# Kernel tuning notes

Hardware: AMD Instinct MI355X
Metric: run time of the kernel (lower is better)

The kernel has to match this reference:

```python
import jax, jax.numpy as jnp
import numpy as np

N, E, G = 50000, 800000, 64
IN_CH, HID, HEADS, NUM_CLASSES = 128, 64, 4, 10
NEG_SLOPE = 0.2


def _gat_conv(x, src, dst, W, a_src, a_dst, b, concat):
    """PyG-style GATConv with default add_self_loops=True (inference mode)."""
    n = x.shape[0]
    H, C = a_src.shape
    h = (x @ W).reshape(n, H, C)                       # [N,H,C]
    loop = jnp.arange(n, dtype=src.dtype)
    si = jnp.concatenate([src, loop])                  # [E+N]
    di = jnp.concatenate([dst, loop])
    as_n = jnp.sum(h * a_src, axis=-1)                 # [N,H]
    ad_n = jnp.sum(h * a_dst, axis=-1)                 # [N,H]
    e = jax.nn.leaky_relu(as_n[si] + ad_n[di], NEG_SLOPE)   # [E+N,H]
    m = jax.ops.segment_max(e, di, num_segments=n)     # segment softmax (stable)
    ex = jnp.exp(e - m[di])
    denom = jax.ops.segment_sum(ex, di, num_segments=n)
    alpha = ex / (denom[di] + 1e-16)                   # [E+N,H]
    out = jax.ops.segment_sum(alpha[:, :, None] * h[si], di, num_segments=n)  # [N,H,C]
    out = out.reshape(n, H * C) if concat else out.mean(axis=1)
    return out + b


def setup_inputs() -> dict:
    key = jax.random.key(0)
    ks = jax.random.split(key, 20)
    d = {}
    d["x"] = jax.random.normal(ks[0], (N, IN_CH), dtype=jnp.float32)
    d["src"] = jax.random.randint(ks[1], (E,), 0, N, dtype=jnp.int32)
    d["dst"] = jax.random.randint(ks[2], (E,), 0, N, dtype=jnp.int32)
    d["batch"] = jnp.sort(jax.random.randint(ks[3], (N,), 0, G, dtype=jnp.int32))
    s = 0.1
    d["W1"] = jax.random.normal(ks[4], (IN_CH, HEADS * HID), dtype=jnp.float32) * s
    d["as1"] = jax.random.normal(ks[5], (HEADS, HID), dtype=jnp.float32) * s
    d["ad1"] = jax.random.normal(ks[6], (HEADS, HID), dtype=jnp.float32) * s
    d["b1"] = jnp.zeros((HEADS * HID,), jnp.float32)
    d["W2"] = jax.random.normal(ks[7], (HEADS * HID, HEADS * HID), dtype=jnp.float32) * s
    d["as2"] = jax.random.normal(ks[8], (HEADS, HID), dtype=jnp.float32) * s
    d["ad2"] = jax.random.normal(ks[9], (HEADS, HID), dtype=jnp.float32) * s
    d["b2"] = jnp.zeros((HEADS * HID,), jnp.float32)
    # proj: 256 -> 64, heads=1, concat=False
    d["Wp"] = jax.random.normal(ks[10], (HEADS * HID, HID), dtype=jnp.float32) * s
    d["asp"] = jax.random.normal(ks[11], (1, HID), dtype=jnp.float32) * s
    d["adp"] = jax.random.normal(ks[12], (1, HID), dtype=jnp.float32) * s
    d["bp"] = jnp.zeros((HID,), jnp.float32)
    # MLP head
    d["Wh1"] = jax.random.normal(ks[13], (HID, HID), dtype=jnp.float32) * s
    d["bh1"] = jnp.zeros((HID,), jnp.float32)
    d["Wh2"] = jax.random.normal(ks[14], (HID, NUM_CLASSES), dtype=jnp.float32) * s
    d["bh2"] = jnp.zeros((NUM_CLASSES,), jnp.float32)
    return d


def reference(x, src, dst, batch, W1, as1, ad1, b1, W2, as2, ad2, b2,
              Wp, asp, adp, bp, Wh1, bh1, Wh2, bh2):
    h = jax.nn.elu(_gat_conv(x, src, dst, W1, as1, ad1, b1, concat=True))
    h = jax.nn.elu(_gat_conv(h, src, dst, W2, as2, ad2, b2, concat=True))
    h = jax.nn.elu(_gat_conv(h, src, dst, Wp, asp, adp, bp, concat=False))  # [N,HID]
    # global mean pool over graphs
    sums = jax.ops.segment_sum(h, batch, num_segments=G)                    # [G,HID]
    cnt = jax.ops.segment_sum(jnp.ones((h.shape[0],), h.dtype), batch, num_segments=G)
    g = sums / jnp.maximum(cnt, 1.0)[:, None]
    z = jax.nn.relu(g @ Wh1 + bh1)
    return z @ Wh2 + bh2                                                    # [G,NUM_CLASSES]
```

## Files before the change

### kernel.cpp

```cpp
#include <hip/hip_runtime.h>
#include <hip/hip_fp16.h>
#include <cstdint>
#include <cstddef>

#define NNODES 50000
#define NEDGES 800000
#define NGRAPH 64
#define BCAP 128

typedef __attribute__((ext_vector_type(8))) _Float16 half8;
typedef __attribute__((ext_vector_type(4))) float float4v;

__device__ __forceinline__ float lrelu(float x) { return x > 0.f ? x : 0.2f * x; }

__device__ __forceinline__ void wtrans_elem(const float* __restrict__ W,
                                            _Float16* __restrict__ Wt,
                                            int K, int N, int i) {
    int k = i / N, n = i - k * N;
    Wt[(size_t)n * K + k] = (_Float16)W[i];
}

__global__ void prep(const float* __restrict__ W1, const float* __restrict__ W2,
                     const float* __restrict__ Wp, _Float16* __restrict__ w1t,
                     _Float16* __restrict__ w2t, _Float16* __restrict__ wpt,
                     int* __restrict__ cnt) {
    int i = blockIdx.x * blockDim.x + threadIdx.x;
    if (i < 32768) wtrans_elem(W1, w1t, 128, 256, i);
    else if (i < 98304) wtrans_elem(W2, w2t, 256, 256, i - 32768);
    else if (i < 114688) wtrans_elem(Wp, wpt, 256, 64, i - 98304);
    else if (i < 114688 + NNODES) cnt[i - 114688] = 0;
}

__global__ __launch_bounds__(256) void scatter(const int* __restrict__ src,
                                               const int* __restrict__ dst,
                                               int* __restrict__ cnt,
                                               int* __restrict__ bucket) {
    int e = blockIdx.x * 256 + threadIdx.x;
    if (e < NEDGES) {
        int d = dst[e];
        int pos = atomicAdd(&cnt[d], 1);
        if (pos < BCAP) bucket[(size_t)d * BCAP + pos] = src[e];
    }
}

template <int KD, int NFB, int NTOT, int HTOT, bool F32A>
__global__ __launch_bounds__(512) void gemm_lds(const _Float16* __restrict__ A,
                                                const float* __restrict__ A32,
                                                const _Float16* __restrict__ Wt,
                                                const float* __restrict__ a_src,
                                                const float* __restrict__ a_dst,
                                                _Float16* __restrict__ C,
                                                float* __restrict__ as_n,
                                                float* __restrict__ ad_n,
                                                int M) {
    constexpr int NSPLIT = NTOT / (NFB * 16);
    constexpr int HLOC = NFB / 4;
    constexpr int KT = KD / 32;
    constexpr int KC = KD / 8;
    extern __shared__ _Float16 bsm[];

    const int bm = blockIdx.x / NSPLIT;
    const int bn = blockIdx.x % NSPLIT;
    const int tid = threadIdx.x;
    const int w = tid >> 6;
    const int lane = tid & 63;
    const int quad = lane >> 4;
    const int mcol = lane & 15;

    int arow = bm * 128 + w * 16 + mcol;
    if (arow >= M) arow = M - 1;

    half8 areg[KT];
    if constexpr (F32A) {
        const float* ap = A32 + (size_t)arow * KD + quad * 8;
#pragma unroll
        for (int i = 0; i < KT; ++i) {
            float4 t0 = *reinterpret_cast<const float4*>(ap + i * 32);
            float4 t1 = *reinterpret_cast<const float4*>(ap + i * 32 + 4);
            areg[i][0] = (_Float16)t0.x; areg[i][1] = (_Float16)t0.y;
            areg[i][2] = (_Float16)t0.z; areg[i][3] = (_Float16)t0.w;
            areg[i][4] = (_Float16)t1.x; areg[i][5] = (_Float16)t1.y;
            areg[i][6] = (_Float16)t1.z; areg[i][7] = (_Float16)t1.w;
        }
    } else {
        const _Float16* ap = A + (size_t)arow * KD + quad * 8;
#pragma unroll
        for (int i = 0; i < KT; ++i)
            areg[i] = *reinterpret_cast<const half8*>(ap + i * 32);
    }

    constexpr int CHUNKS = NFB * 16 * KC;
    const _Float16* wb = Wt + (size_t)bn * NFB * 16 * KD;
#pragma unroll
    for (int it = 0; it < CHUNKS / 512; ++it) {
        int idx = it * 512 + tid;
        int n = idx / KC, c = idx % KC;
        half8 v = *reinterpret_cast<const half8*>(wb + (size_t)n * KD + c * 8);
        *reinterpret_cast<half8*>(&bsm[n * KD + ((c ^ (n & 7)) * 8)]) = v;
    }
    __syncthreads();

    float4v acc[NFB];
#pragma unroll
    for (int nf = 0; nf < NFB; ++nf) acc[nf] = (float4v)0.f;
#pragma unroll
    for (int i = 0; i < KT; ++i) {
#pragma unroll
        for (int nf = 0; nf < NFB; ++nf) {
            int n = nf * 16 + mcol;
            int ch = (quad + i * 4) ^ (n & 7);
            half8 b = *reinterpret_cast<const half8*>(&bsm[n * KD + ch * 8]);
            acc[nf] = __builtin_amdgcn_mfma_f32_16x16x32_f16(areg[i], b, acc[nf], 0, 0, 0);
        }
    }

    const int orow0 = bm * 128 + w * 16 + quad * 4;
    const int cbase = bn * NFB * 16 + mcol;
#pragma unroll
    for (int r = 0; r < 4; ++r) {
        int orow = orow0 + r;
        if (orow < M) {
            _Float16* crow = C + (size_t)orow * NTOT + cbase;
#pragma unroll
            for (int nf = 0; nf < NFB; ++nf) crow[nf * 16] = (_Float16)acc[nf][r];
        }
    }

    float ps[HLOC][4], pd[HLOC][4];
#pragma unroll
    for (int hd = 0; hd < HLOC; ++hd)
#pragma unroll
        for (int r = 0; r < 4; ++r) { ps[hd][r] = 0.f; pd[hd][r] = 0.f; }
#pragma unroll
    for (int nf = 0; nf < NFB; ++nf) {
        float asv = a_src[bn * NFB * 16 + nf * 16 + mcol];
        float adv = a_dst[bn * NFB * 16 + nf * 16 + mcol];
#pragma unroll
        for (int r = 0; r < 4; ++r) {
            ps[nf >> 2][r] = fmaf(acc[nf][r], asv, ps[nf >> 2][r]);
            pd[nf >> 2][r] = fmaf(acc[nf][r], adv, pd[nf >> 2][r]);
        }
    }
#pragma unroll
    for (int off = 1; off < 16; off <<= 1) {
#pragma unroll
        for (int hd = 0; hd < HLOC; ++hd)
#pragma unroll
            for (int r = 0; r < 4; ++r) {
                ps[hd][r] += __shfl_xor(ps[hd][r], off);
                pd[hd][r] += __shfl_xor(pd[hd][r], off);
            }
    }
    if (mcol == 0) {
#pragma unroll
        for (int r = 0; r < 4; ++r) {
            int orow = orow0 + r;
            if (orow < M) {
#pragma unroll
                for (int hd = 0; hd < HLOC; ++hd) {
                    as_n[orow * HTOT + bn * HLOC + hd] = ps[hd][r];
                    ad_n[orow * HTOT + bn * HLOC + hd] = pd[hd][r];
                }
            }
        }
    }
}

__global__ __launch_bounds__(256) void node_agg2(const int* __restrict__ bucket,
                                                 const int* __restrict__ cnt,
                                                 const __half* __restrict__ h,
                                                 const float* __restrict__ asn,
                                                 const float* __restrict__ adn,
                                                 const float* __restrict__ bias,
                                                 _Float16* __restrict__ outp, int Nn) {
    constexpr int H = 4, HC = 256, EPC = 16;
    const int wid = blockIdx.x * 4 + (threadIdx.x >> 6);
    int n0 = wid * 2;
    if (n0 >= Nn) return;
    int n1 = n0 + 1;
    const bool has1 = (n1 < Nn);
    if (!has1) n1 = n0;
    const int lane = threadIdx.x & 63;
    const int hd = lane >> 4;
    const int ej = lane & 15;
    const int base = lane & 48;
    const int rs0 = n0 * BCAP, rs1 = n1 * BCAP;
    const int re0 = rs0 + min(cnt[n0], BCAP);
    const int re1 = rs1 + min(cnt[n1], BCAP);

    const float ad0 = adn[n0 * H + hd];
    const float ad1 = adn[n1 * H + hd];
    const float es0 = lrelu(asn[n0 * H + hd] + ad0);
    const float es1 = lrelu(asn[n1 * H + hd] + ad1);

    float m0 = es0, m1 = es1;
    float dp0 = (ej == 0) ? 1.f : 0.f;
    float dp1 = dp0;

    float a0, a1, a2, a3, b0, b1, b2, b3;
    {
        uint2 u = *reinterpret_cast<const uint2*>(&h[(size_t)n0 * HC + lane * 4]);
        float2 f0 = __half22float2(*reinterpret_cast<__half2*>(&u.x));
        float2 f1 = __half22float2(*reinterpret_cast<__half2*>(&u.y));
        a0 = f0.x; a1 = f0.y; a2 = f1.x; a3 = f1.y;
    }
    {
        uint2 u = *reinterpret_cast<const uint2*>(&h[(size_t)n1 * HC + lane * 4]);
        float2 f0 = __half22float2(*reinterpret_cast<__half2*>(&u.x));
        float2 f1 = __half22float2(*reinterpret_cast<__half2*>(&u.y));
        b0 = f0.x; b1 = f0.y; b2 = f1.x; b3 = f1.y;
    }

    int c0 = rs0, c1 = rs1;
    while (c0 < re0 || c1 < re1) {
        const int i0 = c0 + ej, i1 = c1 + ej;
        int s0v = 0, s1v = 0;
        float e0 = -1e30f, e1 = -1e30f;
        if (i0 < re0) s0v = bucket[i0];
        if (i1 < re1) s1v = bucket[i1];
        if (i0 < re0) e0 = lrelu(asn[s0v * H + hd] + ad0);
        if (i1 < re1) e1 = lrelu(asn[s1v * H + hd] + ad1);

        float cm0 = e0, cm1 = e1;
#pragma unroll
        for (int off = 1; off < EPC; off <<= 1) {
            cm0 = fmaxf(cm0, __shfl_xor(cm0, off));
            cm1 = fmaxf(cm1, __shfl_xor(cm1, off));
        }
        const float mn0 = fmaxf(m0, cm0);
        const float mn1 = fmaxf(m1, cm1);
        const float sc0 = __expf(m0 - mn0);
        const float sc1 = __expf(m1 - mn1);
        m0 = mn0; m1 = mn1;
        dp0 *= sc0; dp1 *= sc1;
        a0 *= sc0; a1 *= sc0; a2 *= sc0; a3 *= sc0;
        b0 *= sc1; b1 *= sc1; b2 *= sc1; b3 *= sc1;
        const float x0 = __expf(e0 - m0);
        const float x1 = __expf(e1 - m1);
        dp0 += x0; dp1 += x1;

        auto bodyA = [&](int j) {
            float ex = __shfl(x0, base + j);
            int sj = __shfl(s0v, base + j);
            uint2 u = *reinterpret_cast<const uint2*>(&h[(size_t)sj * HC + lane * 4]);
            float2 f0 = __half22float2(*reinterpret_cast<__half2*>(&u.x));
            float2 f1 = __half22float2(*reinterpret_cast<__half2*>(&u.y));
            a0 = fmaf(ex, f0.x, a0);
            a1 = fmaf(ex, f0.y, a1);
            a2 = fmaf(ex, f1.x, a2);
            a3 = fmaf(ex, f1.y, a3);
        };
        auto bodyB = [&](int j) {
            float ex = __shfl(x1, base + j);
            int sj = __shfl(s1v, base + j);
            uint2 u = *reinterpret_cast<const uint2*>(&h[(size_t)sj * HC + lane * 4]);
            float2 f0 = __half22float2(*reinterpret_cast<__half2*>(&u.x));
            float2 f1 = __half22float2(*reinterpret_cast<__half2*>(&u.y));
            b0 = fmaf(ex, f0.x, b0);
            b1 = fmaf(ex, f0.y, b1);
            b2 = fmaf(ex, f1.x, b2);
            b3 = fmaf(ex, f1.y, b3);
        };

        const int nA = min(EPC, re0 - c0);
        const int nB = min(EPC, re1 - c1);
        const int nmax = max(nA, nB);
        if (nmax == EPC) {
#pragma unroll
            for (int j = 0; j < EPC; ++j) { bodyA(j); bodyB(j); }
        } else {
#pragma unroll 4
            for (int j = 0; j < nmax; ++j) { bodyA(j); bodyB(j); }
        }
        c0 += EPC; c1 += EPC;
    }

#pragma unroll
    for (int off = 1; off < EPC; off <<= 1) {
        dp0 += __shfl_xor(dp0, off);
        dp1 += __shfl_xor(dp1, off);
    }
    const float inv0 = 1.f / (dp0 + 1e-16f);
    const float inv1 = 1.f / (dp1 + 1e-16f);

    {
        float v0 = a0 * inv0 + bias[lane * 4 + 0];
        float v1 = a1 * inv0 + bias[lane * 4 + 1];
        float v2 = a2 * inv0 + bias[lane * 4 + 2];
        float v3 = a3 * inv0 + bias[lane * 4 + 3];
        v0 = v0 > 0.f ? v0 : expm1f(v0);
        v1 = v1 > 0.f ? v1 : expm1f(v1);
        v2 = v2 > 0.f ? v2 : expm1f(v2);
        v3 = v3 > 0.f ? v3 : expm1f(v3);
        union { _Float16 h4[4]; uint2 u; } r;
        r.h4[0] = (_Float16)v0; r.h4[1] = (_Float16)v1;
        r.h4[2] = (_Float16)v2; r.h4[3] = (_Float16)v3;
        reinterpret_cast<uint2*>(outp + (size_t)n0 * HC)[lane] = r.u;
    }
    if (has1) {
        float v0 = b0 * inv1 + bias[lane * 4 + 0];
        float v1 = b1 * inv1 + bias[lane * 4 + 1];
        float v2 = b2 * inv1 + bias[lane * 4 + 2];
        float v3 = b3 * inv1 + bias[lane * 4 + 3];
        v0 = v0 > 0.f ? v0 : expm1f(v0);
        v1 = v1 > 0.f ? v1 : expm1f(v1);
        v2 = v2 > 0.f ? v2 : expm1f(v2);
        v3 = v3 > 0.f ? v3 : expm1f(v3);
        union { _Float16 h4[4]; uint2 u; } r;
        r.h4[0] = (_Float16)v0; r.h4[1] = (_Float16)v1;
        r.h4[2] = (_Float16)v2; r.h4[3] = (_Float16)v3;
        reinterpret_cast<uint2*>(outp + (size_t)n1 * HC)[lane] = r.u;
    }
}

__global__ __launch_bounds__(256) void node_aggP(const int* __restrict__ bucket,
                                                 const int* __restrict__ cnt,
                                                 const __half* __restrict__ h,
                                                 const float* __restrict__ asn,
                                                 const float* __restrict__ adn,
                                                 const float* __restrict__ bias,
                                                 _Float16* __restrict__ outp, int Nn) {
    constexpr int HC = 64, EPC = 16;
    const int wv = threadIdx.x >> 6;
    const int lane = threadIdx.x & 63;
    const int li = lane & 15;
    const int gb = lane & 48;
    const int n = blockIdx.x * 16 + wv * 4 + (lane >> 4);
    if (n >= Nn) return;

    const int rs = n * BCAP;
    const int re = rs + min(cnt[n], BCAP);
    const float ad = adn[n];
    float m = lrelu(asn[n] + ad);
    float dp = (li == 0) ? 1.f : 0.f;

    float a0, a1, a2, a3;
    {
        uint2 u = *reinterpret_cast<const uint2*>(&h[(size_t)n * HC + li * 4]);
        float2 f0 = __half22float2(*reinterpret_cast<__half2*>(&u.x));
        float2 f1 = __half22float2(*reinterpret_cast<__half2*>(&u.y));
        a0 = f0.x; a1 = f0.y; a2 = f1.x; a3 = f1.y;
    }

    auto body = [&](int j, float x, int sv) {
        float ex = __shfl(x, gb + j);
        int sj = __shfl(sv, gb + j);
        uint2 u = *reinterpret_cast<const uint2*>(&h[(size_t)sj * HC + li * 4]);
        float2 f0 = __half22float2(*reinterpret_cast<__half2*>(&u.x));
        float2 f1 = __half22float2(*reinterpret_cast<__half2*>(&u.y));
        a0 = fmaf(ex, f0.x, a0);
        a1 = fmaf(ex, f0.y, a1);
        a2 = fmaf(ex, f1.x, a2);
        a3 = fmaf(ex, f1.y, a3);
    };

    for (int c = rs; c < re; c += EPC) {
        int i = c + li;
        int sv = 0;
        float e = -1e30f;
        if (i < re) {
            sv = bucket[i];
            e = lrelu(asn[sv] + ad);
        }
        float cm = e;
#pragma unroll
        for (int off = 1; off < EPC; off <<= 1) cm = fmaxf(cm, __shfl_xor(cm, off));
        float mn = fmaxf(m, cm);
        float sc = __expf(m - mn);
        m = mn;
        dp *= sc;
        a0 *= sc; a1 *= sc; a2 *= sc; a3 *= sc;
        float x = __expf(e - m);
        dp += x;
        const int nb2 = min(EPC, re - c);
        if (nb2 == EPC) {
#pragma unroll
            for (int j = 0; j < EPC; ++j) body(j, x, sv);
        } else {
#pragma unroll 4
            for (int j = 0; j < nb2; ++j) body(j, x, sv);
        }
    }
#pragma unroll
    for (int off = 1; off < EPC; off <<= 1) dp += __shfl_xor(dp, off);
    const float inv = 1.f / (dp + 1e-16f);
    float v0 = a0 * inv + bias[li * 4 + 0];
    float v1 = a1 * inv + bias[li * 4 + 1];
    float v2 = a2 * inv + bias[li * 4 + 2];
    float v3 = a3 * inv + bias[li * 4 + 3];
    v0 = v0 > 0.f ? v0 : expm1f(v0);
    v1 = v1 > 0.f ? v1 : expm1f(v1);
    v2 = v2 > 0.f ? v2 : expm1f(v2);
    v3 = v3 > 0.f ? v3 : expm1f(v3);
    union { _Float16 h4[4]; uint2 u; } r;
    r.h4[0] = (_Float16)v0; r.h4[1] = (_Float16)v1;
    r.h4[2] = (_Float16)v2; r.h4[3] = (_Float16)v3;
    *reinterpret_cast<uint2*>(&outp[(size_t)n * HC + li * 4]) = r.u;
}

__global__ __launch_bounds__(256) void pool_mlp(const __half* __restrict__ feat,
                                                const int* __restrict__ batch,
                                                const float* __restrict__ Wh1,
                                                const float* __restrict__ bh1,
                                                const float* __restrict__ Wh2,
                                                const float* __restrict__ bh2,
                                                float* __restrict__ out, int Nn) {
    __shared__ float swsum[4][64];
    __shared__ float smean[64];
    __shared__ float shid[64];
    const int g = blockIdx.x;
    const int tid = threadIdx.x;
    const int lane = tid & 63;
    const int w = tid >> 6;
    int lo = 0, hi = Nn;
    while (lo < hi) { int mid = (lo + hi) >> 1; if (batch[mid] < g) lo = mid + 1; else hi = mid; }
    const int start = lo;
    hi = Nn;
    while (lo < hi) { int mid = (lo + hi) >> 1; if (batch[mid] < g + 1) lo = mid + 1; else hi = mid; }
    const int end = lo;
    float acc = 0.f;
    for (int n = start + w; n < end; n += 4) acc += __half2float(feat[(size_t)n * 64 + lane]);
    swsum[w][lane] = acc;
    __syncthreads();
    if (w == 0) {
        float s = swsum[0][lane] + swsum[1][lane] + swsum[2][lane] + swsum[3][lane];
        float c = (float)(end - start);
        c = c > 1.f ? c : 1.f;
        smean[lane] = s / c;
    }
    __syncthreads();
    if (tid < 64) {
        float a = bh1[tid];
        for (int k = 0; k < 64; ++k) a = fmaf(smean[k], Wh1[k * 64 + tid], a);
        shid[tid] = a > 0.f ? a : 0.f;
    }
    __syncthreads();
    if (tid < 10) {
        float a = bh2[tid];
        for (int k = 0; k < 64; ++k) a = fmaf(shid[k], Wh2[k * 10 + tid], a);
        out[g * 10 + tid] = a;
    }
}

extern "C" void kernel_launch(void* const* d_in, const int* in_sizes, int n_in,
                              void* d_out, int out_size, void* d_ws, size_t ws_size,
                              hipStream_t stream) {
    const float* x   = (const float*)d_in[0];
    const int* src   = (const int*)d_in[1];
    const int* dst   = (const int*)d_in[2];
    const int* batch = (const int*)d_in[3];
    const float* W1  = (const float*)d_in[4];
    const float* as1 = (const float*)d_in[5];
    const float* ad1 = (const float*)d_in[6];
    const float* b1  = (const float*)d_in[7];
    const float* W2  = (const float*)d_in[8];
    const float* as2 = (const float*)d_in[9];
    const float* ad2 = (const float*)d_in[10];
    const float* b2  = (const float*)d_in[11];
    const float* Wp  = (const float*)d_in[12];
    const float* asp = (const float*)d_in[13];
    const float* adp = (const float*)d_in[14];
    const float* bp  = (const float*)d_in[15];
    const float* Wh1 = (const float*)d_in[16];
    const float* bh1 = (const float*)d_in[17];
    const float* Wh2 = (const float*)d_in[18];
    const float* bh2 = (const float*)d_in[19];
    float* out = (float*)d_out;

    _Float16* hbase = (_Float16*)d_ws;
    const size_t NHC = (size_t)NNODES * 256;
    _Float16* ha16  = hbase;
    _Float16* hb16  = ha16 + NHC;
    _Float16* projh = hb16 + NHC;
    _Float16* w1t   = projh + (size_t)NNODES * 64;
    _Float16* w2t   = w1t + 256 * 128;
    _Float16* wpt   = w2t + 256 * 256;
    float* asn = (float*)(wpt + 64 * 256);
    float* adn = asn + (size_t)NNODES * 4;
    int* cnt    = (int*)(adn + (size_t)NNODES * 4);
    int* bucket = cnt + NNODES;

    const int gemmGrid = (NNODES + 127) / 128;
    const int scatGrid = (NEDGES + 255) / 256;
    const int agg2Grid = ((NNODES + 1) / 2 + 3) / 4;
    const int aggPGrid = (NNODES + 15) / 16;

    prep<<<(114688 + NNODES + 255) / 256, 256, 0, stream>>>(W1, W2, Wp, w1t, w2t, wpt, cnt);
    scatter<<<scatGrid, 256, 0, stream>>>(src, dst, cnt, bucket);
    gemm_lds<128, 16, 256, 4, true><<<gemmGrid, 512, 65536, stream>>>(
        nullptr, x, w1t, as1, ad1, ha16, asn, adn, NNODES);
    node_agg2<<<agg2Grid, 256, 0, stream>>>(bucket, cnt,
        (const __half*)ha16, asn, adn, b1, hb16, NNODES);
    gemm_lds<256, 8, 256, 4, false><<<gemmGrid * 2, 512, 65536, stream>>>(
        hb16, nullptr, w2t, as2, ad2, ha16, asn, adn, NNODES);
    node_agg2<<<agg2Grid, 256, 0, stream>>>(bucket, cnt,
        (const __half*)ha16, asn, adn, b2, hb16, NNODES);
    gemm_lds<256, 4, 64, 1, false><<<gemmGrid, 512, 32768, stream>>>(
        hb16, nullptr, wpt, asp, adp, ha16, asn, adn, NNODES);
    node_aggP<<<aggPGrid, 256, 0, stream>>>(bucket, cnt,
        (const __half*)ha16, asn, adn, bp, projh, NNODES);
    pool_mlp<<<NGRAPH, 256, 0, stream>>>((const __half*)projh, batch, Wh1, bh1, Wh2, bh2, out, NNODES);
}
```

Measured before the change: 440.7 us.

## Fuse scatter with weight prep and fuse final aggregation with mean pooling

Merges the weight transpose/convert into the edge-scatter kernel and replaces the cnt-zeroing pass with a memset that also clears a per-graph sum buffer. Fuses the graph mean-pool into the last aggregation kernel through LDS atomics per graph slot, then global atomics, so the fp16 projection output no longer has to be written and re-read. The MLP head then only divides the sums and applies the two layers. This saves a launch and a node-sized round trip, at the cost of fp32 atomics with order-dependent summation.

```diff
diff --git a/kernel.cpp b/kernel.cpp
--- a/kernel.cpp
+++ b/kernel.cpp
@@ -20,26 +20,30 @@
     Wt[(size_t)n * K + k] = (_Float16)W[i];
 }
 
-__global__ void prep(const float* __restrict__ W1, const float* __restrict__ W2,
-                     const float* __restrict__ Wp, _Float16* __restrict__ w1t,
-                     _Float16* __restrict__ w2t, _Float16* __restrict__ wpt,
-                     int* __restrict__ cnt) {
-    int i = blockIdx.x * blockDim.x + threadIdx.x;
-    if (i < 32768) wtrans_elem(W1, w1t, 128, 256, i);
-    else if (i < 98304) wtrans_elem(W2, w2t, 256, 256, i - 32768);
-    else if (i < 114688) wtrans_elem(Wp, wpt, 256, 64, i - 98304);
-    else if (i < 114688 + NNODES) cnt[i - 114688] = 0;
-}
-
-__global__ __launch_bounds__(256) void scatter(const int* __restrict__ src,
-                                               const int* __restrict__ dst,
-                                               int* __restrict__ cnt,
-                                               int* __restrict__ bucket) {
-    int e = blockIdx.x * 256 + threadIdx.x;
-    if (e < NEDGES) {
-        int d = dst[e];
-        int pos = atomicAdd(&cnt[d], 1);
-        if (pos < BCAP) bucket[(size_t)d * BCAP + pos] = src[e];
+#define SCAT_BLOCKS ((NEDGES + 255) / 256)
+
+__global__ __launch_bounds__(256) void scatter_prep(const int* __restrict__ src,
+                                                    const int* __restrict__ dst,
+                                                    int* __restrict__ cnt,
+                                                    int* __restrict__ bucket,
+                                                    const float* __restrict__ W1,
+                                                    const float* __restrict__ W2,
+                                                    const float* __restrict__ Wp,
+                                                    _Float16* __restrict__ w1t,
+                                                    _Float16* __restrict__ w2t,
+                                                    _Float16* __restrict__ wpt) {
+    if ((int)blockIdx.x < SCAT_BLOCKS) {
+        int e = blockIdx.x * 256 + threadIdx.x;
+        if (e < NEDGES) {
+            int d = dst[e];
+            int pos = atomicAdd(&cnt[d], 1);
+            if (pos < BCAP) bucket[(size_t)d * BCAP + pos] = src[e];
+        }
+    } else {
+        int i = (blockIdx.x - SCAT_BLOCKS) * 256 + threadIdx.x;
+        if (i < 32768) wtrans_elem(W1, w1t, 128, 256, i);
+        else if (i < 98304) wtrans_elem(W2, w2t, 256, 256, i - 32768);
+        else if (i < 114688) wtrans_elem(Wp, wpt, 256, 64, i - 98304);
     }
 }
 
@@ -313,123 +317,140 @@
     }
 }
 
-__global__ __launch_bounds__(256) void node_aggP(const int* __restrict__ bucket,
-                                                 const int* __restrict__ cnt,
-                                                 const __half* __restrict__ h,
-                                                 const float* __restrict__ asn,
-                                                 const float* __restrict__ adn,
-                                                 const float* __restrict__ bias,
-                                                 _Float16* __restrict__ outp, int Nn) {
+__global__ __launch_bounds__(256) void node_aggP_pool(const int* __restrict__ bucket,
+                                                      const int* __restrict__ cnt,
+                                                      const __half* __restrict__ h,
+                                                      const float* __restrict__ asn,
+                                                      const float* __restrict__ adn,
+                                                      const float* __restrict__ bias,
+                                                      const int* __restrict__ batch,
+                                                      float* __restrict__ gsum, int Nn) {
     constexpr int HC = 64, EPC = 16;
-    const int wv = threadIdx.x >> 6;
-    const int lane = threadIdx.x & 63;
+    __shared__ float lsum[4][64];
+    __shared__ int lused[4];
+    const int tid = threadIdx.x;
+    lsum[tid >> 6][tid & 63] = 0.f;
+    if (tid < 4) lused[tid] = 0;
+    __syncthreads();
+
+    const int wv = tid >> 6;
+    const int lane = tid & 63;
     const int li = lane & 15;
     const int gb = lane & 48;
-    const int n = blockIdx.x * 16 + wv * 4 + (lane >> 4);
-    if (n >= Nn) return;
-
-    const int rs = n * BCAP;
-    const int re = rs + min(cnt[n], BCAP);
-    const float ad = adn[n];
-    float m = lrelu(asn[n] + ad);
-    float dp = (li == 0) ? 1.f : 0.f;
-
-    float a0, a1, a2, a3;
-    {
-        uint2 u = *reinterpret_cast<const uint2*>(&h[(size_t)n * HC + li * 4]);
-        float2 f0 = __half22float2(*reinterpret_cast<__half2*>(&u.x));
-        float2 f1 = __half22float2(*reinterpret_cast<__half2*>(&u.y));
-        a0 = f0.x; a1 = f0.y; a2 = f1.x; a3 = f1.y;
-    }
-
-    auto body = [&](int j, float x, int sv) {
-        float ex = __shfl(x, gb + j);
-        int sj = __shfl(sv, gb + j);
-        uint2 u = *reinterpret_cast<const uint2*>(&h[(size_t)sj * HC + li * 4]);
-        float2 f0 = __half22float2(*reinterpret_cast<__half2*>(&u.x));
-        float2 f1 = __half22float2(*reinterpret_cast<__half2*>(&u.y));
-        a0 = fmaf(ex, f0.x, a0);
-        a1 = fmaf(ex, f0.y, a1);
-        a2 = fmaf(ex, f1.x, a2);
-        a3 = fmaf(ex, f1.y, a3);
-    };
-
-    for (int c = rs; c < re; c += EPC) {
-        int i = c + li;
-        int sv = 0;
-        float e = -1e30f;
-        if (i < re) {
-            sv = bucket[i];
-            e = lrelu(asn[sv] + ad);
-        }
-        float cm = e;
-#pragma unroll
-        for (int off = 1; off < EPC; off <<= 1) cm = fmaxf(cm, __shfl_xor(cm, off));
-        float mn = fmaxf(m, cm);
-        float sc = __expf(m - mn);
-        m = mn;
-        dp *= sc;
-        a0 *= sc; a1 *= sc; a2 *= sc; a3 *= sc;
-        float x = __expf(e - m);
-        dp += x;
-        const int nb2 = min(EPC, re - c);
-        if (nb2 == EPC) {
-#pragma unroll
-            for (int j = 0; j < EPC; ++j) body(j, x, sv);
+    const int bbase = (int)blockIdx.x * 16;
+    const int n = bbase + wv * 4 + (lane >> 4);
+    const int g0 = batch[bbase < Nn - 1 ? bbase : Nn - 1];
+    const bool active = (n < Nn);
+
+    if (active) {
+        const int rs = n * BCAP;
+        const int re = rs + min(cnt[n], BCAP);
+        const float ad = adn[n];
+        float m = lrelu(asn[n] + ad);
+        float dp = (li == 0) ? 1.f : 0.f;
+
+        float a0, a1, a2, a3;
+        {
+            uint2 u = *reinterpret_cast<const uint2*>(&h[(size_t)n * HC + li * 4]);
+            float2 f0 = __half22float2(*reinterpret_cast<__half2*>(&u.x));
+            float2 f1 = __half22float2(*reinterpret_cast<__half2*>(&u.y));
+            a0 = f0.x; a1 = f0.y; a2 = f1.x; a3 = f1.y;
+        }
+
+        auto body = [&](int j, float x, int sv) {
+            float ex = __shfl(x, gb + j);
+            int sj = __shfl(sv, gb + j);
+            uint2 u = *reinterpret_cast<const uint2*>(&h[(size_t)sj * HC + li * 4]);
+            float2 f0 = __half22float2(*reinterpret_cast<__half2*>(&u.x));
+            float2 f1 = __half22float2(*reinterpret_cast<__half2*>(&u.y));
+            a0 = fmaf(ex, f0.x, a0);
+            a1 = fmaf(ex, f0.y, a1);
+            a2 = fmaf(ex, f1.x, a2);
+            a3 = fmaf(ex, f1.y, a3);
+        };
+
+        for (int c = rs; c < re; c += EPC) {
+            int i = c + li;
+            int sv = 0;
+            float e = -1e30f;
+            if (i < re) {
+                sv = bucket[i];
+                e = lrelu(asn[sv] + ad);
+            }
+            float cm = e;
+#pragma unroll
+            for (int off = 1; off < EPC; off <<= 1) cm = fmaxf(cm, __shfl_xor(cm, off));
+            float mn = fmaxf(m, cm);
+            float sc = __expf(m - mn);
+            m = mn;
+            dp *= sc;
+            a0 *= sc; a1 *= sc; a2 *= sc; a3 *= sc;
+            float x = __expf(e - m);
+            dp += x;
+            const int nb2 = min(EPC, re - c);
+            if (nb2 == EPC) {
+#pragma unroll
+                for (int j = 0; j < EPC; ++j) body(j, x, sv);
+            } else {
+#pragma unroll 4
+                for (int j = 0; j < nb2; ++j) body(j, x, sv);
+            }
+        }
+#pragma unroll
+        for (int off = 1; off < EPC; off <<= 1) dp += __shfl_xor(dp, off);
+        const float inv = 1.f / (dp + 1e-16f);
+        float v0 = a0 * inv + bias[li * 4 + 0];
+        float v1 = a1 * inv + bias[li * 4 + 1];
+        float v2 = a2 * inv + bias[li * 4 + 2];
+        float v3 = a3 * inv + bias[li * 4 + 3];
+        v0 = v0 > 0.f ? v0 : expm1f(v0);
+        v1 = v1 > 0.f ? v1 : expm1f(v1);
+        v2 = v2 > 0.f ? v2 : expm1f(v2);
+        v3 = v3 > 0.f ? v3 : expm1f(v3);
+
+        const int g = batch[n];
+        const int slot = g - g0;
+        if (slot >= 0 && slot < 4) {
+            if (li == 0) lused[slot] = 1;
+            atomicAdd(&lsum[slot][li * 4 + 0], v0);
+            atomicAdd(&lsum[slot][li * 4 + 1], v1);
+            atomicAdd(&lsum[slot][li * 4 + 2], v2);
+            atomicAdd(&lsum[slot][li * 4 + 3], v3);
         } else {
-#pragma unroll 4
-            for (int j = 0; j < nb2; ++j) body(j, x, sv);
-        }
-    }
-#pragma unroll
-    for (int off = 1; off < EPC; off <<= 1) dp += __shfl_xor(dp, off);
-    const float inv = 1.f / (dp + 1e-16f);
-    float v0 = a0 * inv + bias[li * 4 + 0];
-    float v1 = a1 * inv + bias[li * 4 + 1];
-    float v2 = a2 * inv + bias[li * 4 + 2];
-    float v3 = a3 * inv + bias[li * 4 + 3];
-    v0 = v0 > 0.f ? v0 : expm1f(v0);
-    v1 = v1 > 0.f ? v1 : expm1f(v1);
-    v2 = v2 > 0.f ? v2 : expm1f(v2);
-    v3 = v3 > 0.f ? v3 : expm1f(v3);
-    union { _Float16 h4[4]; uint2 u; } r;
-    r.h4[0] = (_Float16)v0; r.h4[1] = (_Float16)v1;
-    r.h4[2] = (_Float16)v2; r.h4[3] = (_Float16)v3;
-    *reinterpret_cast<uint2*>(&outp[(size_t)n * HC + li * 4]) = r.u;
-}
-
-__global__ __launch_bounds__(256) void pool_mlp(const __half* __restrict__ feat,
-                                                const int* __restrict__ batch,
-                                                const float* __restrict__ Wh1,
-                                                const float* __restrict__ bh1,
-                                                const float* __restrict__ Wh2,
-                                                const float* __restrict__ bh2,
-                                                float* __restrict__ out, int Nn) {
-    __shared__ float swsum[4][64];
+            atomicAdd(&gsum[g * 64 + li * 4 + 0], v0);
+            atomicAdd(&gsum[g * 64 + li * 4 + 1], v1);
+            atomicAdd(&gsum[g * 64 + li * 4 + 2], v2);
+            atomicAdd(&gsum[g * 64 + li * 4 + 3], v3);
+        }
+    }
+    __syncthreads();
+    const int slot = tid >> 6, ch = tid & 63;
+    if (lused[slot] && g0 + slot < NGRAPH)
+        atomicAdd(&gsum[(g0 + slot) * 64 + ch], lsum[slot][ch]);
+}
+
+__global__ __launch_bounds__(64) void mlp_head(const float* __restrict__ gsum,
+                                               const int* __restrict__ batch,
+                                               const float* __restrict__ Wh1,
+                                               const float* __restrict__ bh1,
+                                               const float* __restrict__ Wh2,
+                                               const float* __restrict__ bh2,
+                                               float* __restrict__ out, int Nn) {
     __shared__ float smean[64];
     __shared__ float shid[64];
     const int g = blockIdx.x;
     const int tid = threadIdx.x;
-    const int lane = tid & 63;
-    const int w = tid >> 6;
     int lo = 0, hi = Nn;
     while (lo < hi) { int mid = (lo + hi) >> 1; if (batch[mid] < g) lo = mid + 1; else hi = mid; }
     const int start = lo;
     hi = Nn;
     while (lo < hi) { int mid = (lo + hi) >> 1; if (batch[mid] < g + 1) lo = mid + 1; else hi = mid; }
     const int end = lo;
-    float acc = 0.f;
-    for (int n = start + w; n < end; n += 4) acc += __half2float(feat[(size_t)n * 64 + lane]);
-    swsum[w][lane] = acc;
+    float c = (float)(end - start);
+    c = c > 1.f ? c : 1.f;
+    smean[tid] = gsum[g * 64 + tid] / c;
     __syncthreads();
-    if (w == 0) {
-        float s = swsum[0][lane] + swsum[1][lane] + swsum[2][lane] + swsum[3][lane];
-        float c = (float)(end - start);
-        c = c > 1.f ? c : 1.f;
-        smean[lane] = s / c;
-    }
-    __syncthreads();
-    if (tid < 64) {
+    {
         float a = bh1[tid];
         for (int k = 0; k < 64; ++k) a = fmaf(smean[k], Wh1[k * 64 + tid], a);
         shid[tid] = a > 0.f ? a : 0.f;
@@ -471,22 +492,23 @@
     const size_t NHC = (size_t)NNODES * 256;
     _Float16* ha16  = hbase;
     _Float16* hb16  = ha16 + NHC;
-    _Float16* projh = hb16 + NHC;
-    _Float16* w1t   = projh + (size_t)NNODES * 64;
+    _Float16* w1t   = hb16 + NHC;
     _Float16* w2t   = w1t + 256 * 128;
     _Float16* wpt   = w2t + 256 * 256;
     float* asn = (float*)(wpt + 64 * 256);
     float* adn = asn + (size_t)NNODES * 4;
     int* cnt    = (int*)(adn + (size_t)NNODES * 4);
-    int* bucket = cnt + NNODES;
+    float* gsum = (float*)(cnt + NNODES);
+    int* bucket = (int*)(gsum + NGRAPH * 64);
 
     const int gemmGrid = (NNODES + 127) / 128;
-    const int scatGrid = (NEDGES + 255) / 256;
+    const int prepBlocks = (114688 + 255) / 256;
     const int agg2Grid = ((NNODES + 1) / 2 + 3) / 4;
     const int aggPGrid = (NNODES + 15) / 16;
 
-    prep<<<(114688 + NNODES + 255) / 256, 256, 0, stream>>>(W1, W2, Wp, w1t, w2t, wpt, cnt);
-    scatter<<<scatGrid, 256, 0, stream>>>(src, dst, cnt, bucket);
+    (void)hipMemsetAsync(cnt, 0, (size_t)NNODES * 4 + (size_t)NGRAPH * 64 * 4, stream);
+    scatter_prep<<<SCAT_BLOCKS + prepBlocks, 256, 0, stream>>>(
+        src, dst, cnt, bucket, W1, W2, Wp, w1t, w2t, wpt);
     gemm_lds<128, 16, 256, 4, true><<<gemmGrid, 512, 65536, stream>>>(
         nullptr, x, w1t, as1, ad1, ha16, asn, adn, NNODES);
     node_agg2<<<agg2Grid, 256, 0, stream>>>(bucket, cnt,
@@ -497,7 +519,7 @@
         (const __half*)ha16, asn, adn, b2, hb16, NNODES);
     gemm_lds<256, 4, 64, 1, false><<<gemmGrid, 512, 32768, stream>>>(
         hb16, nullptr, wpt, asp, adp, ha16, asn, adn, NNODES);
-    node_aggP<<<aggPGrid, 256, 0, stream>>>(bucket, cnt,
-        (const __half*)ha16, asn, adn, bp, projh, NNODES);
-    pool_mlp<<<NGRAPH, 256, 0, stream>>>((const __half*)projh, batch, Wh1, bh1, Wh2, bh2, out, NNODES);
-}
+    node_aggP_pool<<<aggPGrid, 256, 0, stream>>>(bucket, cnt,
+        (const __half*)ha16, asn, adn, bp, batch, gsum, NNODES);
+    mlp_head<<<NGRAPH, 64, 0, stream>>>(gsum, batch, Wh1, bh1, Wh2, bh2, out, NNODES);
+}
```

After: 412.4 us. 1.07x faster.
